# Kernel optimization log

Hardware: AMD Instinct MI355X
Metric: run time of the kernel (lower is better)

Reference implementation:

```python
import jax, jax.numpy as jnp
import numpy as np

B, LQ, LKV = 4, 512, 8192
Q_DIM, KV_DIM = 1024, 512
QK_CH, V_CH, N_HEADS = 256, 256, 8
EPS = 1e-5


def _layernorm(x, g, b):
    m = jnp.mean(x, axis=-1, keepdims=True)
    v = jnp.mean(jnp.square(x - m), axis=-1, keepdims=True)
    return (x - m) * jax.lax.rsqrt(v + EPS) * g + b


def setup_inputs() -> dict:
    key = jax.random.key(0)
    ks = jax.random.split(key, 8)
    hidden_states = jax.random.normal(ks[0], (B, LQ, Q_DIM), dtype=jnp.float32)
    inputs = jax.random.normal(ks[1], (B, LKV, KV_DIM), dtype=jnp.float32)
    # Linear weights stored as [in, out] for x @ W
    Wq = jax.random.normal(ks[2], (Q_DIM, QK_CH), dtype=jnp.float32) * (1.0 / np.sqrt(Q_DIM))
    Wk = jax.random.normal(ks[3], (KV_DIM, QK_CH), dtype=jnp.float32) * (1.0 / np.sqrt(KV_DIM))
    Wv = jax.random.normal(ks[4], (KV_DIM, V_CH), dtype=jnp.float32) * (1.0 / np.sqrt(KV_DIM))
    bq = jnp.zeros((QK_CH,), jnp.float32)
    bk = jax.random.normal(ks[5], (QK_CH,), dtype=jnp.float32) * 0.02
    bv = jax.random.normal(ks[6], (V_CH,), dtype=jnp.float32) * 0.02
    ln1_g = jnp.ones((Q_DIM,), jnp.float32)
    ln1_b = jnp.zeros((Q_DIM,), jnp.float32)
    ln2_g = jnp.ones((KV_DIM,), jnp.float32)
    ln2_b = jnp.zeros((KV_DIM,), jnp.float32)
    return dict(hidden_states=hidden_states, inputs=inputs,
                ln1_g=ln1_g, ln1_b=ln1_b, ln2_g=ln2_g, ln2_b=ln2_b,
                Wq=Wq, bq=bq, Wk=Wk, bk=bk, Wv=Wv, bv=bv)


def reference(hidden_states, inputs, ln1_g, ln1_b, ln2_g, ln2_b,
              Wq, bq, Wk, bk, Wv, bv):
    H = N_HEADS
    dqk = QK_CH // H
    dv = V_CH // H
    hs = _layernorm(hidden_states, ln1_g, ln1_b)          # [B,LQ,Q_DIM]
    inp = _layernorm(inputs, ln2_g, ln2_b)                # [B,LKV,KV_DIM]
    q = (hs @ Wq + bq).reshape(B, LQ, H, dqk)             # [B,LQ,H,dqk]
    k = (inp @ Wk + bk).reshape(B, LKV, H, dqk)           # [B,LKV,H,dqk]
    v = (inp @ Wv + bv).reshape(B, LKV, H, dv)            # [B,LKV,H,dv]
    scores = jnp.einsum('bqhd,bkhd->bhqk', q, k) / np.sqrt(dqk).astype(np.float32)
    probs = jax.nn.softmax(scores, axis=-1)               # [B,H,LQ,LKV] (materialized, as in torch)
    ctx = jnp.einsum('bhqk,bkhd->bqhd', probs, v)         # [B,LQ,H,dv]
    return ctx.reshape(B, LQ, H * dv)
```

## Files before the change

kernel.cpp:

```cpp
#include <hip/hip_runtime.h>
#include <hip/hip_bf16.h>
#include <math.h>

#define NB    4
#define LQ    512
#define LKV   8192
#define QDIM  1024
#define KVDIM 512
#define NH    8
#define EPS_LN 1e-5f
#define SMAX  12.0f

typedef __attribute__((ext_vector_type(8))) short bf16x8;
typedef __attribute__((ext_vector_type(4))) float f32x4;

static __device__ __forceinline__ ushort f2bf(float x) {
    unsigned int u = __builtin_bit_cast(unsigned int, x);
    u += 0x7FFFu + ((u >> 16) & 1u);
    return (ushort)(u >> 16);
}

#if __has_builtin(__builtin_amdgcn_cvt_pk_bf16_f32)
static __device__ __forceinline__ unsigned int pk_bf16(float a, float b) {
    auto r = __builtin_amdgcn_cvt_pk_bf16_f32(a, b);
    return __builtin_bit_cast(unsigned int, r);
}
#else
static __device__ __forceinline__ unsigned int pk_bf16(float a, float b) {
    return (unsigned int)f2bf(a) | ((unsigned int)f2bf(b) << 16);
}
#endif

#if __has_builtin(__builtin_amdgcn_exp2f)
#define EXP2F(x) __builtin_amdgcn_exp2f(x)
#else
#define EXP2F(x) exp2f(x)
#endif

static __device__ __forceinline__ void interleave_swap(unsigned int &x, unsigned int &y, int lane) {
#if __has_builtin(__builtin_amdgcn_permlane32_swap) && __has_builtin(__builtin_amdgcn_permlane16_swap)
    {
        auto r1 = __builtin_amdgcn_permlane32_swap(x, y, false, false);
        auto r2 = __builtin_amdgcn_permlane16_swap(r1[0], r1[1], false, false);
        x = (unsigned int)r2[0];
        y = (unsigned int)r2[1];
    }
#else
    {
        unsigned int xs = (unsigned int)__shfl_xor((int)x, 32, 64);
        unsigned int ys = (unsigned int)__shfl_xor((int)y, 32, 64);
        unsigned int A2 = (lane & 32) ? ys : x;
        unsigned int C2 = (lane & 32) ? y  : xs;
        unsigned int A2x = (unsigned int)__shfl_xor((int)A2, 16, 64);
        unsigned int C2x = (unsigned int)__shfl_xor((int)C2, 16, 64);
        x = (lane & 16) ? C2x : A2;
        y = (lane & 16) ? C2  : A2x;
    }
#endif
}

static __device__ __forceinline__ void gld_lds16(const ushort* g, ushort* l) {
    __builtin_amdgcn_global_load_lds(
        (const __attribute__((address_space(1))) unsigned int*)g,
        (__attribute__((address_space(3))) unsigned int*)l, 16, 0, 0);
}

template<int K>
static __device__ __forceinline__ void ln_norm_row(
    const float* __restrict__ x, const float* __restrict__ g,
    const float* __restrict__ bta, ushort* __restrict__ y, int row, int lane)
{
    const float* xp = x + (size_t)row * K;
    constexpr int NV = K / 256;
    float4 v[NV];
    float s = 0.f;
#pragma unroll
    for (int i = 0; i < NV; ++i) {
        v[i] = *(const float4*)(xp + lane * 4 + i * 256);
        s += v[i].x + v[i].y + v[i].z + v[i].w;
    }
#pragma unroll
    for (int o = 1; o < 64; o <<= 1) s += __shfl_xor(s, o, 64);
    const float mu = s * (1.0f / K);
    float vs = 0.f;
#pragma unroll
    for (int i = 0; i < NV; ++i) {
        float dx = v[i].x - mu, dy = v[i].y - mu, dz = v[i].z - mu, dw = v[i].w - mu;
        vs += dx * dx + dy * dy + dz * dz + dw * dw;
    }
#pragma unroll
    for (int o = 1; o < 64; o <<= 1) vs += __shfl_xor(vs, o, 64);
    const float rs = rsqrtf(vs * (1.0f / K) + EPS_LN);
#pragma unroll
    for (int i = 0; i < NV; ++i) {
        const float4 gv = *(const float4*)(g   + lane * 4 + i * 256);
        const float4 bv = *(const float4*)(bta + lane * 4 + i * 256);
        uint2 o;
        o.x = pk_bf16((v[i].x - mu) * rs * gv.x + bv.x, (v[i].y - mu) * rs * gv.y + bv.y);
        o.y = pk_bf16((v[i].z - mu) * rs * gv.z + bv.z, (v[i].w - mu) * rs * gv.w + bv.w);
        *(uint2*)(y + (size_t)row * K + lane * 4 + i * 256) = o;
    }
}

static __device__ __forceinline__ void ln_stats_row(
    const float* __restrict__ x, float* __restrict__ mean, float* __restrict__ rstd,
    int row, int lane)
{
    const float* xp = x + (size_t)row * QDIM;
    float4 v[4];
    float s = 0.f;
#pragma unroll
    for (int i = 0; i < 4; ++i) {
        v[i] = *(const float4*)(xp + lane * 4 + i * 256);
        s += v[i].x + v[i].y + v[i].z + v[i].w;
    }
#pragma unroll
    for (int o = 1; o < 64; o <<= 1) s += __shfl_xor(s, o, 64);
    const float mu = s * (1.0f / QDIM);
    float vs = 0.f;
#pragma unroll
    for (int i = 0; i < 4; ++i) {
        float dx = v[i].x - mu, dy = v[i].y - mu, dz = v[i].z - mu, dw = v[i].w - mu;
        vs += dx * dx + dy * dy + dz * dz + dw * dw;
    }
#pragma unroll
    for (int o = 1; o < 64; o <<= 1) vs += __shfl_xor(vs, o, 64);
    if (lane == 0) {
        mean[row] = mu;
        rstd[row] = rsqrtf(vs * (1.0f / QDIM) + EPS_LN);
    }
}

static __device__ __forceinline__ void wt_transpose_body(
    const float* __restrict__ src, ushort* __restrict__ dst, int K,
    int kx, int ny, int t, ushort (*Ts)[72])
{
    const int k0 = kx * 64, n0 = ny * 64;
    const int nl = t & 63;
#pragma unroll
    for (int p = 0; p < 16; ++p) {
        const int kl = p * 4 + (t >> 6);
        Ts[nl][kl] = f2bf(src[(size_t)(k0 + kl) * 256 + n0 + nl]);
    }
    __syncthreads();
    const int ck = (t & 7) * 8;
#pragma unroll
    for (int p = 0; p < 2; ++p) {
        const int rn = p * 32 + (t >> 3);
        *(bf16x8*)(dst + (size_t)(n0 + rn) * K + k0 + ck) = *(const bf16x8*)&Ts[rn][ck];
    }
}

__global__ __launch_bounds__(256) void phaseA_kernel(
    const float* __restrict__ inputs, const float* __restrict__ ln2g,
    const float* __restrict__ ln2b,   ushort* __restrict__ Abf,
    const float* __restrict__ hidden, float* __restrict__ mean_h, float* __restrict__ rstd_h,
    const float* __restrict__ Wq, const float* __restrict__ Wk, const float* __restrict__ Wv,
    ushort* __restrict__ WtQ, ushort* __restrict__ WtKV)
{
    __shared__ ushort Ts[64][72];
    const int bid = blockIdx.x;
    const int t = threadIdx.x;
    const int lane = t & 63;
    if (bid < 8192) {
        ln_norm_row<KVDIM>(inputs, ln2g, ln2b, Abf, bid * 4 + (t >> 6), lane);
    } else if (bid < 8704) {
        ln_stats_row(hidden, mean_h, rstd_h, (bid - 8192) * 4 + (t >> 6), lane);
    } else if (bid < 8768) {
        const int p = bid - 8704;
        wt_transpose_body(Wq, WtQ, QDIM, p & 15, p >> 4, t, Ts);
    } else if (bid < 8800) {
        const int p = bid - 8768;
        wt_transpose_body(Wk, WtKV, KVDIM, p & 7, p >> 3, t, Ts);
    } else {
        const int p = bid - 8800;
        wt_transpose_body(Wv, WtKV + (size_t)256 * KVDIM, KVDIM, p & 7, p >> 3, t, Ts);
    }
}

__global__ __launch_bounds__(256) void phaseB_kernel(
    const ushort* __restrict__ Abf, const ushort* __restrict__ WtKV,
    const float* __restrict__ bk, const float* __restrict__ bv,
    ushort* __restrict__ kb, ushort* __restrict__ vt,
    const float* __restrict__ hidden, const float* __restrict__ mean_h,
    const float* __restrict__ rstd_h,
    const float* __restrict__ ln1g, const float* __restrict__ ln1b,
    const ushort* __restrict__ WtQ, const float* __restrict__ bq,
    ushort* __restrict__ qb, float oscale)
{
    __shared__ __align__(16) ushort SMEM[4 * 64 * 72];
    const int bid  = blockIdx.x;
    const int t    = threadIdx.x;
    const int lane = t & 63;
    const int w    = t >> 6;
    const int lq   = lane & 15;
    const int lg   = lane >> 4;
    const int wm   = w >> 1;
    const int wn   = w & 1;

    if (bid < 1024) {
        const int bm = (bid >> 2) * 128;
        const int bn = (bid & 3) * 128;
        ushort* As = SMEM;
        ushort* Bs = SMEM + 4096;

        const int srow = t >> 2;
        const int scol = ((t & 3) ^ ((t >> 3) & 3)) * 8;
        const ushort* gA = Abf  + (size_t)(bm + srow) * KVDIM + scol;
        const ushort* gB = WtKV + (size_t)(bn + srow) * KVDIM + scol;
        ushort* lA = As + t * 8;
        ushort* lB = Bs + t * 8;

        f32x4 acc[4][4] = {};
        for (int k0 = 0; k0 < KVDIM; k0 += 32) {
            gld_lds16(gA + k0,                       lA);
            gld_lds16(gA + (size_t)64 * KVDIM + k0,  lA + 2048);
            gld_lds16(gB + k0,                       lB);
            gld_lds16(gB + (size_t)64 * KVDIM + k0,  lB + 2048);
            __syncthreads();
            bf16x8 af[4], bf[4];
#pragma unroll
            for (int mt = 0; mt < 4; ++mt) {
                const int m = wm * 64 + mt * 16 + lq;
                af[mt] = *(const bf16x8*)(As + m * 32 + ((lg ^ ((m >> 1) & 3)) << 3));
            }
#pragma unroll
            for (int nt = 0; nt < 4; ++nt) {
                const int n = wn * 64 + nt * 16 + lq;
                bf[nt] = *(const bf16x8*)(Bs + n * 32 + ((lg ^ ((n >> 1) & 3)) << 3));
            }
#pragma unroll
            for (int mt = 0; mt < 4; ++mt)
#pragma unroll
                for (int nt = 0; nt < 4; ++nt)
                    acc[mt][nt] = __builtin_amdgcn_mfma_f32_16x16x32_bf16(af[mt], bf[nt], acc[mt][nt], 0, 0, 0);
            __syncthreads();
        }
        const int m0base = bm + wm * 64;
        const int bidx   = m0base >> 13;
        const int tokb   = m0base & 8191;

        if (bn < 256) {
            ushort (*Cs)[72] = (ushort(*)[72])(SMEM + w * 64 * 72);
#pragma unroll
            for (int nt = 0; nt < 4; ++nt) {
                const int n_l = nt * 16 + lq;
                const float bias = bk[bn + wn * 64 + n_l];
#pragma unroll
                for (int mt = 0; mt < 4; ++mt)
#pragma unroll
                    for (int r = 0; r < 4; ++r)
                        Cs[mt * 16 + lg * 4 + r][n_l] = f2bf(acc[mt][nt][r] + bias);
            }
            const int r0 = lane >> 3;
            const int ck = (lane & 7) * 8;
            const int nc = bn + wn * 64 + ck;
            const int h = nc >> 5, d = nc & 31;
            const size_t obase = (((size_t)(bidx * NH + h) << 13) + tokb) * 32 + d;
#pragma unroll
            for (int p = 0; p < 8; ++p) {
                const int row = p * 8 + r0;
                *(bf16x8*)(kb + obase + (size_t)row * 32) = *(const bf16x8*)&Cs[row][ck];
            }
        } else {
            ushort (*Cs)[72] = (ushort(*)[72])(SMEM + w * 64 * 72);
#pragma unroll
            for (int nt = 0; nt < 4; ++nt) {
                const int n_l = nt * 16 + lq;
                const float bias = bv[(bn - 256) + wn * 64 + n_l];
#pragma unroll
                for (int mt = 0; mt < 4; ++mt) {
                    uint2 o;
                    o.x = pk_bf16(acc[mt][nt][0] + bias, acc[mt][nt][1] + bias);
                    o.y = pk_bf16(acc[mt][nt][2] + bias, acc[mt][nt][3] + bias);
                    *(uint2*)&Cs[n_l][mt * 16 + lg * 4] = o;
                }
            }
            const int r0 = lane >> 3;
            const int cm = (lane & 7) * 8;
            const int tokc = tokb + cm;
#pragma unroll
            for (int p = 0; p < 8; ++p) {
                const int row = p * 8 + r0;
                const int nv  = (bn - 256) + wn * 64 + row;
                const int h = nv >> 5, d = nv & 31;
                *(bf16x8*)(vt + ((size_t)(bidx * NH + h) * 32 + d) * LKV + tokc) =
                    *(const bf16x8*)&Cs[row][cm];
            }
        }
    } else {
        const int p  = bid - 1024;
        const int bm = (p >> 2) * 64;
        const int bn = (p & 3) * 64;
        ushort* As = SMEM;
        ushort* Bs = SMEM + 4096;

        const int srow = t >> 3;
        const int scol = ((t & 7) ^ (srow & 7)) * 8;
        const ushort* gB = WtQ + (size_t)(bn + srow) * QDIM + scol;
        ushort* lB  = Bs + t * 8;
        ushort* lA0 = As + t * 8;
        ushort* lA1 = As + 2048 + t * 8;

        const int r0 = bm + srow;
        const float mu0 = mean_h[r0],      rs0 = rstd_h[r0];
        const float mu1 = mean_h[r0 + 32], rs1 = rstd_h[r0 + 32];
        const float* xA0 = hidden + (size_t)r0 * QDIM + scol;
        const float* xA1 = xA0 + (size_t)32 * QDIM;

        f32x4 acc[2][2] = {};
        for (int k0 = 0; k0 < QDIM; k0 += 64) {
            gld_lds16(gB + k0,                      lB);
            gld_lds16(gB + (size_t)32 * QDIM + k0,  lB + 2048);
            const float4 a0 = *(const float4*)(xA0 + k0);
            const float4 a1 = *(const float4*)(xA0 + k0 + 4);
            const float4 c0 = *(const float4*)(xA1 + k0);
            const float4 c1 = *(const float4*)(xA1 + k0 + 4);
            const float4 g0 = *(const float4*)(ln1g + k0 + scol);
            const float4 g1 = *(const float4*)(ln1g + k0 + scol + 4);
            const float4 d0 = *(const float4*)(ln1b + k0 + scol);
            const float4 d1 = *(const float4*)(ln1b + k0 + scol + 4);
            uint4 w0, w1;
            w0.x = pk_bf16((a0.x - mu0) * rs0 * g0.x + d0.x, (a0.y - mu0) * rs0 * g0.y + d0.y);
            w0.y = pk_bf16((a0.z - mu0) * rs0 * g0.z + d0.z, (a0.w - mu0) * rs0 * g0.w + d0.w);
            w0.z = pk_bf16((a1.x - mu0) * rs0 * g1.x + d1.x, (a1.y - mu0) * rs0 * g1.y + d1.y);
            w0.w = pk_bf16((a1.z - mu0) * rs0 * g1.z + d1.z, (a1.w - mu0) * rs0 * g1.w + d1.w);
            w1.x = pk_bf16((c0.x - mu1) * rs1 * g0.x + d0.x, (c0.y - mu1) * rs1 * g0.y + d0.y);
            w1.y = pk_bf16((c0.z - mu1) * rs1 * g0.z + d0.z, (c0.w - mu1) * rs1 * g0.w + d0.w);
            w1.z = pk_bf16((c1.x - mu1) * rs1 * g1.x + d1.x, (c1.y - mu1) * rs1 * g1.y + d1.y);
            w1.w = pk_bf16((c1.z - mu1) * rs1 * g1.z + d1.z, (c1.w - mu1) * rs1 * g1.w + d1.w);
            *(uint4*)lA0 = w0;
            *(uint4*)lA1 = w1;
            __syncthreads();
#pragma unroll
            for (int kh = 0; kh < 2; ++kh) {
                bf16x8 af[2], bf[2];
#pragma unroll
                for (int mt = 0; mt < 2; ++mt) {
                    const int m = wm * 32 + mt * 16 + lq;
                    af[mt] = *(const bf16x8*)(As + m * 64 + (((lg + 4 * kh) ^ (m & 7)) << 3));
                }
#pragma unroll
                for (int nt = 0; nt < 2; ++nt) {
                    const int n = wn * 32 + nt * 16 + lq;
                    bf[nt] = *(const bf16x8*)(Bs + n * 64 + (((lg + 4 * kh) ^ (n & 7)) << 3));
                }
#pragma unroll
                for (int mt = 0; mt < 2; ++mt)
#pragma unroll
                    for (int nt = 0; nt < 2; ++nt)
                        acc[mt][nt] = __builtin_amdgcn_mfma_f32_16x16x32_bf16(af[mt], bf[nt], acc[mt][nt], 0, 0, 0);
            }
            __syncthreads();
        }

#pragma unroll
        for (int nt = 0; nt < 2; ++nt) {
            const int n = bn + wn * 32 + nt * 16 + lq;
            const int h = n >> 5, d = n & 31;
            const float bias = bq[n];
#pragma unroll
            for (int mt = 0; mt < 2; ++mt) {
                const int m0   = bm + wm * 32 + mt * 16 + lg * 4;
                const int bidx = m0 >> 9;
                const int tok  = m0 & 511;
                const size_t base = (((size_t)(bidx * NH + h) << 9) + tok) * 32 + d;
#pragma unroll
                for (int r = 0; r < 4; ++r)
                    qb[base + (size_t)r * 32] = f2bf((acc[mt][nt][r] + bias) * oscale);
            }
        }
    }
}

__global__ __launch_bounds__(512, 4) void attn_mfma_kernel(
    const ushort* __restrict__ Qb,
    const ushort* __restrict__ Kb,
    const ushort* __restrict__ Vt,
    float* __restrict__ Out)
{
    const int bid = blockIdx.x;
    const int xcd = bid & 7;
    const int rr  = bid >> 3;
    const int bh  = ((rr & 3) << 3) | xcd;
    const int qt  = rr >> 2;
    const int b = bh >> 3, h = bh & 7;
    const int t = threadIdx.x, w = t >> 6, lane = t & 63;
    const int lq = lane & 15, lg = lane >> 4;

    __shared__ __align__(16) float Ob[4 * 32 * 36];
    __shared__ float lbuf[8][32];

    bf16x8 qfrag[2];
    const size_t qbase = ((size_t)bh * LQ + qt * 32) * 32;
    qfrag[0] = *(const bf16x8*)(Qb + qbase + (size_t)lq * 32 + lg * 8);
    qfrag[1] = *(const bf16x8*)(Qb + qbase + (size_t)(16 + lq) * 32 + lg * 8);

    const ushort* KpA = Kb + ((size_t)bh * LKV + w * 1024 + lq) * 32 + lg * 8;
    const ushort* VpA = Vt + ((size_t)bh * 32 + lq) * LKV + w * 1024 + lg * 8;

    f32x4 oacc[2][2] = {};
    float l_part[2] = {0.f, 0.f};
    const f32x4 cM = {-SMAX, -SMAX, -SMAX, -SMAX};

    bf16x8 kf[4];
#pragma unroll
    for (int m = 0; m < 4; ++m)
        kf[m] = *(const bf16x8*)(KpA + (size_t)(m * 16) * 32);

    for (int kt = 0; kt < 1024; kt += 64) {
        bf16x8 kc[4];
#pragma unroll
        for (int m = 0; m < 4; ++m) kc[m] = kf[m];

        bf16x8 vc[2][2];
#pragma unroll
        for (int dt = 0; dt < 2; ++dt)
#pragma unroll
            for (int hf = 0; hf < 2; ++hf)
                vc[dt][hf] = *(const bf16x8*)(VpA + (size_t)(dt * 16) * LKV + kt + hf * 32);

        const int nk = (kt + 64 < 1024) ? kt + 64 : 0;
#pragma unroll
        for (int m = 0; m < 4; ++m)
            kf[m] = *(const bf16x8*)(KpA + (size_t)(nk + m * 16) * 32);

        f32x4 s[4][2];
#pragma unroll
        for (int m = 0; m < 4; ++m)
#pragma unroll
            for (int n = 0; n < 2; ++n)
                s[m][n] = __builtin_amdgcn_mfma_f32_16x16x32_bf16(kc[m], qfrag[n], cM, 0, 0, 0);

        bf16x8 pf[2][2];
#pragma unroll
        for (int n = 0; n < 2; ++n) {
#pragma unroll
            for (int z = 0; z < 2; ++z) {
                const float e0 = EXP2F(s[2 * z][n][0]);
                const float e1 = EXP2F(s[2 * z][n][1]);
                const float e2 = EXP2F(s[2 * z][n][2]);
                const float e3 = EXP2F(s[2 * z][n][3]);
                const float f0 = EXP2F(s[2 * z + 1][n][0]);
                const float f1 = EXP2F(s[2 * z + 1][n][1]);
                const float f2 = EXP2F(s[2 * z + 1][n][2]);
                const float f3 = EXP2F(s[2 * z + 1][n][3]);
                l_part[n] += ((e0 + e1) + (e2 + e3)) + ((f0 + f1) + (f2 + f3));
                unsigned int wa = pk_bf16(e0, e1);
                unsigned int wb = pk_bf16(e2, e3);
                unsigned int wc = pk_bf16(f0, f1);
                unsigned int wd = pk_bf16(f2, f3);
                interleave_swap(wa, wc, lane);
                interleave_swap(wb, wd, lane);
                uint4 wv;
                wv.x = wa; wv.y = wb; wv.z = wc; wv.w = wd;
                pf[n][z] = __builtin_bit_cast(bf16x8, wv);
            }
        }

#pragma unroll
        for (int dt = 0; dt < 2; ++dt)
#pragma unroll
            for (int n = 0; n < 2; ++n) {
                oacc[dt][n] = __builtin_amdgcn_mfma_f32_16x16x32_bf16(vc[dt][0], pf[n][0], oacc[dt][n], 0, 0, 0);
                oacc[dt][n] = __builtin_amdgcn_mfma_f32_16x16x32_bf16(vc[dt][1], pf[n][1], oacc[dt][n], 0, 0, 0);
            }
    }

#pragma unroll
    for (int n = 0; n < 2; ++n) {
        l_part[n] += __shfl_xor(l_part[n], 16);
        l_part[n] += __shfl_xor(l_part[n], 32);
    }
    if (lg == 0) {
        lbuf[w][lq]      = l_part[0];
        lbuf[w][16 + lq] = l_part[1];
    }
    if (w >= 4) {
#pragma unroll
        for (int n = 0; n < 2; ++n)
#pragma unroll
            for (int dt = 0; dt < 2; ++dt)
                *(f32x4*)&Ob[((size_t)(w - 4) * 32 + n * 16 + lq) * 36 + dt * 16 + lg * 4] = oacc[dt][n];
    }
    __syncthreads();
    if (w < 4) {
#pragma unroll
        for (int n = 0; n < 2; ++n)
#pragma unroll
            for (int dt = 0; dt < 2; ++dt) {
                float* p = &Ob[((size_t)w * 32 + n * 16 + lq) * 36 + dt * 16 + lg * 4];
                f32x4 v = *(f32x4*)p;
                v += oacc[dt][n];
                *(f32x4*)p = v;
            }
    }
    __syncthreads();
    {
        const int q  = t >> 4;
        const int d0 = (t & 15) * 2;
        float s0 = 0.f, s1 = 0.f;
#pragma unroll
        for (int j = 0; j < 4; ++j) {
            s0 += Ob[((size_t)j * 32 + q) * 36 + d0];
            s1 += Ob[((size_t)j * 32 + q) * 36 + d0 + 1];
        }
        float gl = 0.f;
#pragma unroll
        for (int j = 0; j < 8; ++j) gl += lbuf[j][q];
        const float inv = 1.0f / gl;
        float2 o; o.x = s0 * inv; o.y = s1 * inv;
        *(float2*)(Out + ((size_t)b * LQ + qt * 32 + q) * 256 + h * 32 + d0) = o;
    }
}

extern "C" void kernel_launch(void* const* d_in, const int* in_sizes, int n_in,
                              void* d_out, int out_size, void* d_ws, size_t ws_size,
                              hipStream_t stream)
{
    const float* hidden = (const float*)d_in[0];
    const float* inputs = (const float*)d_in[1];
    const float* ln1g   = (const float*)d_in[2];
    const float* ln1b   = (const float*)d_in[3];
    const float* ln2g   = (const float*)d_in[4];
    const float* ln2b   = (const float*)d_in[5];
    const float* Wq     = (const float*)d_in[6];
    const float* bq     = (const float*)d_in[7];
    const float* Wk     = (const float*)d_in[8];
    const float* bk     = (const float*)d_in[9];
    const float* Wv     = (const float*)d_in[10];
    const float* bv     = (const float*)d_in[11];
    float* out = (float*)d_out;

    char* wsb = (char*)d_ws;
    ushort* qb     = (ushort*)(wsb);
    ushort* WtKV   = (ushort*)(wsb + (1u << 20));
    ushort* WtQ    = (ushort*)(wsb + (1u << 20) + (512u << 10));
    float*  mean_h = (float*)(wsb + (2u << 20));
    float*  rstd_h = (float*)(wsb + (2u << 20) + 8192);
    ushort* kb     = (ushort*)(wsb + (2u << 20) + 16384);
    ushort* vt     = (ushort*)(wsb + (18u << 20) + 16384);
    ushort* Abf    = (ushort*)(wsb + (34u << 20) + 16384);

    const float oscale = 0.2550540226496112f;

    phaseA_kernel<<<8832, 256, 0, stream>>>(inputs, ln2g, ln2b, Abf,
                                            hidden, mean_h, rstd_h,
                                            Wq, Wk, Wv, WtQ, WtKV);
    phaseB_kernel<<<1152, 256, 0, stream>>>(Abf, WtKV, bk, bv, kb, vt,
                                            hidden, mean_h, rstd_h, ln1g, ln1b,
                                            WtQ, bq, qb, oscale);
    attn_mfma_kernel<<<512, 512, 0, stream>>>(qb, kb, vt, out);
}
```

Before: 213.6 us.

## Split attention KV range across two blocks and add a combine kernel

The attention kernel now splits the 8192-long KV sequence into two halves handled by separate blocks, doubling the grid from 512 to 1024 blocks. Each block writes unnormalized partial outputs and row sums to workspace, which reuses the Abf buffer. A new combine kernel adds the two partials and normalizes. The aim is better CU occupancy on a 256-CU part, at the cost of an extra launch and partial-result traffic to global memory.

After: 216.1 us. No clear change (+1.2%).

```diff
diff --git a/kernel.cpp b/kernel.cpp
--- a/kernel.cpp
+++ b/kernel.cpp
@@ -377,14 +377,15 @@
     const ushort* __restrict__ Qb,
     const ushort* __restrict__ Kb,
     const ushort* __restrict__ Vt,
-    float* __restrict__ Out)
+    float* __restrict__ Opart,
+    float* __restrict__ lpart)
 {
     const int bid = blockIdx.x;
     const int xcd = bid & 7;
     const int rr  = bid >> 3;
     const int bh  = ((rr & 3) << 3) | xcd;
-    const int qt  = rr >> 2;
-    const int b = bh >> 3, h = bh & 7;
+    const int qt  = (rr >> 2) & 15;
+    const int half = rr >> 6;
     const int t = threadIdx.x, w = t >> 6, lane = t & 63;
     const int lq = lane & 15, lg = lane >> 4;
 
@@ -396,8 +397,9 @@
     qfrag[0] = *(const bf16x8*)(Qb + qbase + (size_t)lq * 32 + lg * 8);
     qfrag[1] = *(const bf16x8*)(Qb + qbase + (size_t)(16 + lq) * 32 + lg * 8);
 
-    const ushort* KpA = Kb + ((size_t)bh * LKV + w * 1024 + lq) * 32 + lg * 8;
-    const ushort* VpA = Vt + ((size_t)bh * 32 + lq) * LKV + w * 1024 + lg * 8;
+    const int kv0 = half * 4096 + w * 512;
+    const ushort* KpA = Kb + ((size_t)bh * LKV + kv0 + lq) * 32 + lg * 8;
+    const ushort* VpA = Vt + ((size_t)bh * 32 + lq) * LKV + kv0 + lg * 8;
 
     f32x4 oacc[2][2] = {};
     float l_part[2] = {0.f, 0.f};
@@ -408,7 +410,7 @@
     for (int m = 0; m < 4; ++m)
         kf[m] = *(const bf16x8*)(KpA + (size_t)(m * 16) * 32);
 
-    for (int kt = 0; kt < 1024; kt += 64) {
+    for (int kt = 0; kt < 512; kt += 64) {
         bf16x8 kc[4];
 #pragma unroll
         for (int m = 0; m < 4; ++m) kc[m] = kf[m];
@@ -420,7 +422,7 @@
             for (int hf = 0; hf < 2; ++hf)
                 vc[dt][hf] = *(const bf16x8*)(VpA + (size_t)(dt * 16) * LKV + kt + hf * 32);
 
-        const int nk = (kt + 64 < 1024) ? kt + 64 : 0;
+        const int nk = (kt + 64 < 512) ? kt + 64 : 0;
 #pragma unroll
         for (int m = 0; m < 4; ++m)
             kf[m] = *(const bf16x8*)(KpA + (size_t)(nk + m * 16) * 32);
@@ -497,6 +499,7 @@
     }
     __syncthreads();
     {
+        const int pidx = (half * 32 + bh) * 16 + qt;
         const int q  = t >> 4;
         const int d0 = (t & 15) * 2;
         float s0 = 0.f, s1 = 0.f;
@@ -505,13 +508,40 @@
             s0 += Ob[((size_t)j * 32 + q) * 36 + d0];
             s1 += Ob[((size_t)j * 32 + q) * 36 + d0 + 1];
         }
-        float gl = 0.f;
-#pragma unroll
-        for (int j = 0; j < 8; ++j) gl += lbuf[j][q];
-        const float inv = 1.0f / gl;
-        float2 o; o.x = s0 * inv; o.y = s1 * inv;
-        *(float2*)(Out + ((size_t)b * LQ + qt * 32 + q) * 256 + h * 32 + d0) = o;
-    }
+        float2 o; o.x = s0; o.y = s1;
+        *(float2*)(Opart + (size_t)pidx * 1024 + q * 32 + d0) = o;
+        if ((t & 15) == 0) {
+            float gl = 0.f;
+#pragma unroll
+            for (int j = 0; j < 8; ++j) gl += lbuf[j][q];
+            lpart[(size_t)pidx * 32 + q] = gl;
+        }
+    }
+}
+
+__global__ __launch_bounds__(256) void attn_combine_kernel(
+    const float* __restrict__ Opart, const float* __restrict__ lpart,
+    float* __restrict__ Out)
+{
+    const int cb = blockIdx.x;
+    const int bh = cb >> 4, qt = cb & 15;
+    const int b = bh >> 3, h = bh & 7;
+    const int t = threadIdx.x;
+    const int q = t >> 3;
+    const int dq = (t & 7) * 4;
+    const size_t i0 = ((size_t)(bh * 16 + qt)) * 1024 + q * 32 + dq;
+    const size_t i1 = ((size_t)((32 + bh) * 16 + qt)) * 1024 + q * 32 + dq;
+    const float4 a = *(const float4*)(Opart + i0);
+    const float4 c = *(const float4*)(Opart + i1);
+    const float l = lpart[(size_t)(bh * 16 + qt) * 32 + q]
+                  + lpart[(size_t)((32 + bh) * 16 + qt) * 32 + q];
+    const float inv = 1.0f / l;
+    float4 o;
+    o.x = (a.x + c.x) * inv;
+    o.y = (a.y + c.y) * inv;
+    o.z = (a.z + c.z) * inv;
+    o.w = (a.w + c.w) * inv;
+    *(float4*)(Out + ((size_t)b * LQ + qt * 32 + q) * 256 + h * 32 + dq) = o;
 }
 
 extern "C" void kernel_launch(void* const* d_in, const int* in_sizes, int n_in,
@@ -542,6 +572,9 @@
     ushort* vt     = (ushort*)(wsb + (18u << 20) + 16384);
     ushort* Abf    = (ushort*)(wsb + (34u << 20) + 16384);
 
+    float* Opart = (float*)Abf;
+    float* lpart = Opart + (size_t)2 * 32 * 16 * 1024;
+
     const float oscale = 0.2550540226496112f;
 
     phaseA_kernel<<<8832, 256, 0, stream>>>(inputs, ln2g, ln2b, Abf,
@@ -550,5 +583,6 @@
     phaseB_kernel<<<1152, 256, 0, stream>>>(Abf, WtKV, bk, bv, kb, vt,
                                             hidden, mean_h, rstd_h, ln1g, ln1b,
                                             WtQ, bq, qb, oscale);
-    attn_mfma_kernel<<<512, 512, 0, stream>>>(qb, kb, vt, out);
-}
+    attn_mfma_kernel<<<1024, 512, 0, stream>>>(qb, kb, vt, Opart, lpart);
+    attn_combine_kernel<<<512, 256, 0, stream>>>(Opart, lpart, out);
+}
```
